# Kernel tuning notes

Hardware: AMD Instinct MI355X
Metric: run time of the kernel (lower is better)

The kernel has to match this reference:

```python
import jax, jax.numpy as jnp
import numpy as np

B, L, DIN, DM, NL, DI, DS, DC, DTR, NC = 32, 1024, 9, 512, 4, 1024, 16, 4, 32, 12


def setup_inputs() -> dict:
    key = jax.random.key(0)
    ks = jax.random.split(key, 8)
    s = 0.02
    return {
        'x': jax.random.normal(ks[0], (B, L, DIN), jnp.float32),
        'ip_w': jax.random.normal(ks[1], (DM, DIN), jnp.float32) * s,
        'ip_b': jnp.zeros((DM,), jnp.float32),
        'ln_g': jnp.ones((NL, DM), jnp.float32),
        'ln_b': jnp.zeros((NL, DM), jnp.float32),
        'in_proj_w': jax.random.normal(ks[2], (NL, 2 * DI, DM), jnp.float32) * s,
        'conv_w': jax.random.normal(ks[3], (NL, DI, DC), jnp.float32) * s,
        'conv_b': jnp.zeros((NL, DI), jnp.float32),
        'x_proj_w': jax.random.normal(ks[4], (NL, DTR + 2 * DS, DI), jnp.float32) * s,
        'dt_w': jax.random.normal(ks[5], (NL, DI, DTR), jnp.float32) * s,
        'dt_b': jnp.zeros((NL, DI), jnp.float32),
        'A_log': jnp.tile(jnp.log(jnp.arange(1, DS + 1, dtype=jnp.float32))[None, None, :], (NL, DI, 1)),
        'D': jnp.ones((NL, DI), jnp.float32),
        'out_proj_w': jax.random.normal(ks[6], (NL, DM, DI), jnp.float32) * s,
        'fc_w': jax.random.normal(ks[7], (NC, DM), jnp.float32) * s,
        'fc_b': jnp.zeros((NC,), jnp.float32),
    }


def _layernorm(x, g, b):
    m = jnp.mean(x, axis=-1, keepdims=True)
    v = jnp.var(x, axis=-1, keepdims=True)
    return (x - m) * jax.lax.rsqrt(v + 1e-5) * g + b


def _mamba(x, in_w, cw, cb, xp_w, dtw, dtb, Alog, Dp, ow):
    # x: (B, L, DM)
    xz = jnp.einsum('bld,ed->ble', x, in_w)          # (B, L, 2*DI)
    u, z = jnp.split(xz, 2, axis=-1)
    # causal depthwise conv1d over time
    ut = jnp.transpose(u, (0, 2, 1))                  # (B, DI, L)
    ut = jnp.pad(ut, ((0, 0), (0, 0), (DC - 1, 0)))
    conv = jax.lax.conv_general_dilated(
        ut, cw[:, None, :], (1,), 'VALID',
        feature_group_count=DI, dimension_numbers=('NCH', 'OIH', 'NCH'))
    u = jax.nn.silu(jnp.transpose(conv + cb[None, :, None], (0, 2, 1)))  # (B, L, DI)
    x_dbl = jnp.einsum('ble,fe->blf', u, xp_w)        # (B, L, DTR+2*DS)
    dt, Bm, Cm = jnp.split(x_dbl, [DTR, DTR + DS], axis=-1)
    delta = jax.nn.softplus(jnp.einsum('blr,er->ble', dt, dtw) + dtb)    # (B, L, DI)
    A = -jnp.exp(Alog)                                # (DI, DS)

    def step(h, inp):
        d_t, B_t, C_t, u_t = inp                      # (B,DI) (B,DS) (B,DS) (B,DI)
        dA = jnp.exp(d_t[:, :, None] * A)             # (B, DI, DS)
        h = dA * h + (d_t * u_t)[:, :, None] * B_t[:, None, :]
        y = jnp.einsum('bes,bs->be', h, C_t)
        return h, y

    xs = (jnp.moveaxis(delta, 1, 0), jnp.moveaxis(Bm, 1, 0),
          jnp.moveaxis(Cm, 1, 0), jnp.moveaxis(u, 1, 0))
    h0 = jnp.zeros((x.shape[0], DI, DS), x.dtype)
    _, ys = jax.lax.scan(step, h0, xs)                # (L, B, DI)
    y = jnp.moveaxis(ys, 0, 1) + u * Dp
    y = y * jax.nn.silu(z)
    return jnp.einsum('ble,de->bld', y, ow)           # (B, L, DM)


def reference(x, ip_w, ip_b, ln_g, ln_b, in_proj_w, conv_w, conv_b, x_proj_w, dt_w, dt_b, A_log, D, out_proj_w, fc_w, fc_b):
    h = jnp.einsum('bli,di->bld', x, ip_w) + ip_b
    for i in range(NL):
        res = h
        hn = _layernorm(h, ln_g[i], ln_b[i])
        h = _mamba(hn, in_proj_w[i], conv_w[i], conv_b[i], x_proj_w[i],
                   dt_w[i], dt_b[i], A_log[i], D[i], out_proj_w[i]) + res
    pooled = jnp.mean(h, axis=1)                      # (B, DM); dropout is identity in eval
    return pooled @ fc_w.T + fc_b                     # (B, NC)
```

## Files before the change

### kernel.cpp

```cpp
#include <hip/hip_runtime.h>
#include <hip/hip_bf16.h>

#define B_   32
#define L_   1024
#define DIN_ 9
#define DM_  512
#define NL_  4
#define DI_  1024
#define DS_  16
#define DC_  4
#define DTR_ 32
#define NC_  12
#define M_   (B_*L_)
#define NCC_ 2
#define MC_  (M_/NCC_)
#define BC_  (B_/NCC_)
#define NCH_ 16
#define CHT_ 64

typedef unsigned short u16;
typedef __attribute__((ext_vector_type(8))) short bf16x8;
typedef __attribute__((ext_vector_type(4))) float f32x4;

__device__ __forceinline__ float bf2f(u16 h){
  union { unsigned int u; float f; } v; v.u = ((unsigned int)h) << 16; return v.f;
}
__device__ __forceinline__ u16 f2bf(float f){
  union { float f; unsigned int u; } v; v.f = f;
  unsigned int u = v.u;
  return (u16)((u + 0x7fffu + ((u >> 16) & 1u)) >> 16);
}
__device__ __forceinline__ float siluf(float x){ return x / (1.f + __expf(-x)); }

__device__ __forceinline__ void gload_lds16(const u16* g, u16* l){
  __builtin_amdgcn_global_load_lds(
      (const __attribute__((address_space(1))) void*)(unsigned long long)(const void*)g,
      (__attribute__((address_space(3))) void*)(unsigned int)(unsigned long long)(void*)l,
      16, 0, 0);
}

#define NW1_ (NL_*2*DI_*DM_)
#define NW3_ (NL_*DM_*DI_)
#define NW2_ (NL_*64*DI_)
#define NW4_ (NL_*DI_*DTR_)
__global__ __launch_bounds__(256) void cast4_kernel(const float* __restrict__ a,
                                                    const float* __restrict__ c,
                                                    const float* __restrict__ e,
                                                    const float* __restrict__ f,
                                                    u16* __restrict__ oa,
                                                    u16* __restrict__ oc,
                                                    u16* __restrict__ oe,
                                                    u16* __restrict__ of){
  int i = blockIdx.x * 256 + threadIdx.x;
  if (i < NW1_) oa[i] = f2bf(a[i]);
  else if (i < NW1_ + NW3_) oc[i - NW1_] = f2bf(c[i - NW1_]);
  else if (i < NW1_ + NW3_ + NW2_) oe[i - NW1_ - NW3_] = f2bf(e[i - NW1_ - NW3_]);
  else if (i < NW1_ + NW3_ + NW2_ + NW4_)
    of[i - NW1_ - NW3_ - NW2_] = f2bf(f[i - NW1_ - NW3_ - NW2_]);
}

__global__ __launch_bounds__(256) void prep_kernel(const float* __restrict__ convw,
                                                   const float* __restrict__ A_log,
                                                   float* __restrict__ cwt,
                                                   float* __restrict__ At){
  int gid = blockIdx.x * 256 + threadIdx.x;
  int l = gid >> 10, e = gid & (DI_ - 1);
  float4 cw = *(const float4*)(convw + (size_t)gid * 4);
  cwt[(l * 4 + 0) * DI_ + e] = cw.x;
  cwt[(l * 4 + 1) * DI_ + e] = cw.y;
  cwt[(l * 4 + 2) * DI_ + e] = cw.z;
  cwt[(l * 4 + 3) * DI_ + e] = cw.w;
  const float* ar = A_log + (size_t)gid * DS_;
#pragma unroll
  for (int s = 0; s < DS_; s++)
    At[((size_t)l * DS_ + s) * DI_ + e] = -__expf(ar[s]);
}

__global__ __launch_bounds__(512) void inproj_kernel(const float* __restrict__ x,
                                                     const float* __restrict__ w,
                                                     const float* __restrict__ bias,
                                                     u16* __restrict__ h){
  int m = blockIdx.x;
  int d = threadIdx.x;
  __shared__ float xr[DIN_];
  if (threadIdx.x < DIN_) xr[threadIdx.x] = x[(size_t)m * DIN_ + threadIdx.x];
  __syncthreads();
  float a = bias[d];
#pragma unroll
  for (int i = 0; i < DIN_; i++) a += xr[i] * w[d * DIN_ + i];
  h[(size_t)m * DM_ + d] = f2bf(a);
}

__global__ __launch_bounds__(256) void ln_kernel(const u16* __restrict__ h,
                                                 const float* __restrict__ g,
                                                 const float* __restrict__ bt,
                                                 u16* __restrict__ hn){
  int row = blockIdx.x * 4 + (threadIdx.x >> 6);
  int lane = threadIdx.x & 63;
  const u16* hr = h + (size_t)row * DM_ + lane * 8;
  ushort4 a0 = *(const ushort4*)(hr);
  ushort4 a1 = *(const ushort4*)(hr + 4);
  float v[8];
  v[0]=bf2f(a0.x); v[1]=bf2f(a0.y); v[2]=bf2f(a0.z); v[3]=bf2f(a0.w);
  v[4]=bf2f(a1.x); v[5]=bf2f(a1.y); v[6]=bf2f(a1.z); v[7]=bf2f(a1.w);
  float s = 0.f, q = 0.f;
#pragma unroll
  for (int i = 0; i < 8; i++){ s += v[i]; q += v[i]*v[i]; }
#pragma unroll
  for (int o = 32; o; o >>= 1){ s += __shfl_xor(s, o); q += __shfl_xor(q, o); }
  float mean = s * (1.f / DM_);
  float rstd = rsqrtf(q * (1.f / DM_) - mean * mean + 1e-5f);
  float4 g0 = *(const float4*)(g + lane * 8);
  float4 g1 = *(const float4*)(g + lane * 8 + 4);
  float4 b0 = *(const float4*)(bt + lane * 8);
  float4 b1 = *(const float4*)(bt + lane * 8 + 4);
  ushort4 o0, o1;
  o0.x = f2bf((v[0]-mean)*rstd*g0.x + b0.x);
  o0.y = f2bf((v[1]-mean)*rstd*g0.y + b0.y);
  o0.z = f2bf((v[2]-mean)*rstd*g0.z + b0.z);
  o0.w = f2bf((v[3]-mean)*rstd*g0.w + b0.w);
  o1.x = f2bf((v[4]-mean)*rstd*g1.x + b1.x);
  o1.y = f2bf((v[5]-mean)*rstd*g1.y + b1.y);
  o1.z = f2bf((v[6]-mean)*rstd*g1.z + b1.z);
  o1.w = f2bf((v[7]-mean)*rstd*g1.w + b1.w);
  u16* op = hn + (size_t)row * DM_ + lane * 8;
  *(ushort4*)(op)     = o0;
  *(ushort4*)(op + 4) = o1;
}

__global__ __launch_bounds__(256) void conv8_kernel(const u16* __restrict__ xu,
                                                    const float* __restrict__ cwt,
                                                    const float* __restrict__ cbp,
                                                    u16* __restrict__ ub){
  int idx = blockIdx.x * 256 + threadIdx.x;
  int e8 = (idx & 127) * 8;
  int bl = idx >> 7;
  int l = bl & (L_ - 1);
  const u16* p = xu + (size_t)bl * DI_ + e8;
  float acc[8];
  {
    float4 c0 = *(const float4*)(cbp + e8);
    float4 c1 = *(const float4*)(cbp + e8 + 4);
    acc[0]=c0.x; acc[1]=c0.y; acc[2]=c0.z; acc[3]=c0.w;
    acc[4]=c1.x; acc[5]=c1.y; acc[6]=c1.z; acc[7]=c1.w;
  }
#pragma unroll
  for (int d = 0; d < 4; d++){
    if (l - 3 + d >= 0){
      const u16* q = p - (size_t)(3 - d) * DI_;
      ushort4 v0 = *(const ushort4*)q, v1 = *(const ushort4*)(q + 4);
      float4 w0 = *(const float4*)(cwt + d * DI_ + e8);
      float4 w1 = *(const float4*)(cwt + d * DI_ + e8 + 4);
      acc[0] += bf2f(v0.x) * w0.x; acc[1] += bf2f(v0.y) * w0.y;
      acc[2] += bf2f(v0.z) * w0.z; acc[3] += bf2f(v0.w) * w0.w;
      acc[4] += bf2f(v1.x) * w1.x; acc[5] += bf2f(v1.y) * w1.y;
      acc[6] += bf2f(v1.z) * w1.z; acc[7] += bf2f(v1.w) * w1.w;
    }
  }
  ushort4 h0, h1;
  h0.x = f2bf(siluf(acc[0])); h0.y = f2bf(siluf(acc[1]));
  h0.z = f2bf(siluf(acc[2])); h0.w = f2bf(siluf(acc[3]));
  h1.x = f2bf(siluf(acc[4])); h1.y = f2bf(siluf(acc[5]));
  h1.z = f2bf(siluf(acc[6])); h1.w = f2bf(siluf(acc[7]));
  u16* o = ub + (size_t)bl * DI_ + e8;
  *(ushort4*)o = h0;
  *(ushort4*)(o + 4) = h1;
}

template<int BM, int BN, int BK, int EPI>
__global__ __launch_bounds__(256)
void gemm_bt(const u16* __restrict__ A, int lda,
             const u16* __restrict__ Bw,
             u16* Cb, u16* Cb2, const u16* Res,
             const float* __restrict__ bias,
             int N, int K, int nsplit, int gx){
  constexpr int CH = BK / 8;
  constexpr int MASK = CH - 1;
  constexpr int WM = BM / 2, WN = BN / 2;
  constexpr int FM = WM / 16, FN = WN / 16;
  __shared__ u16 As_[BM * BK];
  __shared__ u16 Bs_[BN * BK];
  const int tid = threadIdx.x;
  const int lane = tid & 63;
  const int wid = tid >> 6;
  const int wr = wid >> 1, wc = wid & 1;
  int bm, bn;
  {
    const int wg = blockIdx.x;
    const int gy = (int)gridDim.x / gx;
    const int ypx = gy >> 3;
    const int xcd = wg & 7;
    const int idx = wg >> 3;
    const int y = xcd * ypx + (idx % ypx);
    const int x = idx / ypx;
    bm = y * BM; bn = x * BN;
  }
  f32x4 acc[FM][FN];
#pragma unroll
  for (int i = 0; i < FM; i++)
#pragma unroll
    for (int j = 0; j < FN; j++) acc[i][j] = f32x4{0.f, 0.f, 0.f, 0.f};
  constexpr int LA = BM * BK / (256 * 8);
  constexpr int LB = BN * BK / (256 * 8);
  const int wbase = wid * 64;
  for (int k0 = 0; k0 < K; k0 += BK){
    __syncthreads();
#pragma unroll
    for (int i = 0; i < LA; i++){
      int chunk = i * 256 + tid;
      int row = chunk / CH, cs = chunk & MASK;
      int cg = cs ^ (row & MASK);
      const u16* g = A + (size_t)(bm + row) * lda + k0 + cg * 8;
      gload_lds16(g, &As_[(i * 256 + wbase) * 8]);
    }
#pragma unroll
    for (int i = 0; i < LB; i++){
      int chunk = i * 256 + tid;
      int row = chunk / CH, cs = chunk & MASK;
      int cg = cs ^ (row & MASK);
      const u16* g = Bw + (size_t)(bn + row) * K + k0 + cg * 8;
      gload_lds16(g, &Bs_[(i * 256 + wbase) * 8]);
    }
    __syncthreads();
#pragma unroll
    for (int kk = 0; kk < BK / 32; kk++){
      bf16x8 af[FM], bfr[FN];
      const int kch = kk * 4 + (lane >> 4);
#pragma unroll
      for (int mi = 0; mi < FM; mi++){
        int r = wr * WM + mi * 16 + (lane & 15);
        af[mi] = *(const bf16x8*)(&As_[r * BK + ((kch ^ (r & MASK))) * 8]);
      }
#pragma unroll
      for (int ni = 0; ni < FN; ni++){
        int r = wc * WN + ni * 16 + (lane & 15);
        bfr[ni] = *(const bf16x8*)(&Bs_[r * BK + ((kch ^ (r & MASK))) * 8]);
      }
#pragma unroll
      for (int mi = 0; mi < FM; mi++)
#pragma unroll
        for (int ni = 0; ni < FN; ni++)
          acc[mi][ni] = __builtin_amdgcn_mfma_f32_16x16x32_bf16(af[mi], bfr[ni], acc[mi][ni], 0, 0, 0);
    }
  }
  const int rq = (lane >> 4) * 4, cl = lane & 15;
#pragma unroll
  for (int mi = 0; mi < FM; mi++){
#pragma unroll
    for (int ni = 0; ni < FN; ni++){
      const int n = bn + wc * WN + ni * 16 + cl;
#pragma unroll
      for (int j = 0; j < 4; j++){
        const int m = bm + wr * WM + mi * 16 + rq + j;
        float v = acc[mi][ni][j];
        if constexpr (EPI == 0){
          Cb[(size_t)m * N + n] = f2bf(v);
        } else if constexpr (EPI == 1){
          float xx = v + bias[n];
          float sp = (xx > 20.f) ? xx : __logf(1.f + __expf(xx));
          Cb[(size_t)m * N + n] = f2bf(sp);
        } else if constexpr (EPI == 2){
          const size_t off = (size_t)m * N + n;
          Cb[off] = f2bf(v + bf2f(Res[off]));
        } else {
          if (n < nsplit){
            Cb[(size_t)m * nsplit + n] = f2bf(v);
          } else {
            Cb2[(size_t)m * nsplit + (n - nsplit)] = f2bf(siluf(v));
          }
        }
      }
    }
  }
}

__global__ __launch_bounds__(256)
void scan1_kernel(const u16* __restrict__ ub, const u16* __restrict__ dlt,
                  const u16* __restrict__ xdb,
                  const float* __restrict__ At, float* __restrict__ sb){
  const int tid = threadIdx.x;
  const int e = blockIdx.x * 256 + tid;
  const int c = blockIdx.y, b = blockIdx.z;
  __shared__ float Bsh[CHT_][DS_];
  {
    int row = tid >> 2, col4 = (tid & 3) * 4;
    const u16* p = xdb + ((size_t)b * L_ + (size_t)c * CHT_ + row) * 64 + 32 + col4;
    ushort4 v = *(const ushort4*)p;
    Bsh[row][col4+0] = bf2f(v.x); Bsh[row][col4+1] = bf2f(v.y);
    Bsh[row][col4+2] = bf2f(v.z); Bsh[row][col4+3] = bf2f(v.w);
  }
  __syncthreads();
  float As[DS_];
  bool fast = true;
#pragma unroll
  for (int s = 0; s < DS_; s++){
    As[s] = At[(size_t)s * DI_ + e];
    fast = fast && (fabsf(As[s] + (float)(s + 1)) <= 1e-3f * (s + 1));
  }
  float h[DS_];
#pragma unroll
  for (int s = 0; s < DS_; s++) h[s] = 0.f;
  float sdd = 0.f;
  const size_t base = ((size_t)b * L_ + (size_t)c * CHT_) * DI_ + e;
  if (fast){
    for (int t = 0; t < CHT_; t++){
      const size_t idx = base + (size_t)t * DI_;
      float ut = bf2f(ub[idx]);
      float delta = bf2f(dlt[idx]);
      sdd += delta;
      float du = delta * ut;
      float e1 = __expf(-delta);
      float e2 = e1*e1, e4 = e2*e2, e8 = e4*e4;
      float dA[DS_] = {e1, e2, e2*e1, e4, e4*e1, e4*e2, e4*e2*e1, e8,
                       e8*e1, e8*e2, e8*e2*e1, e8*e4, e8*e4*e1, e8*e4*e2,
                       e8*e4*e2*e1, e8*e8};
      const float* r = &Bsh[t][0];
#pragma unroll
      for (int s = 0; s < DS_; s++)
        h[s] = fmaf(dA[s], h[s], du * r[s]);
    }
  } else {
    for (int t = 0; t < CHT_; t++){
      const size_t idx = base + (size_t)t * DI_;
      float ut = bf2f(ub[idx]);
      float delta = bf2f(dlt[idx]);
      sdd += delta;
      float du = delta * ut;
      const float* r = &Bsh[t][0];
#pragma unroll
      for (int s = 0; s < DS_; s++)
        h[s] = fmaf(__expf(delta * As[s]), h[s], du * r[s]);
    }
  }
  float* p = sb + ((size_t)c * (BC_ * DI_) + (size_t)b * DI_ + e) * 32;
  if (fast){
    float e1 = __expf(-sdd);
    float e2 = e1*e1, e4 = e2*e2, e8 = e4*e4;
    float ap[DS_] = {e1, e2, e2*e1, e4, e4*e1, e4*e2, e4*e2*e1, e8,
                     e8*e1, e8*e2, e8*e2*e1, e8*e4, e8*e4*e1, e8*e4*e2,
                     e8*e4*e2*e1, e8*e8};
#pragma unroll
    for (int s = 0; s < DS_; s++) p[s] = ap[s];
  } else {
#pragma unroll
    for (int s = 0; s < DS_; s++) p[s] = __expf(As[s] * sdd);
  }
#pragma unroll
  for (int s = 0; s < DS_; s++) p[16 + s] = h[s];
}

__global__ __launch_bounds__(256)
void scan2_kernel(float* __restrict__ sb){
  const int be = blockIdx.x * 256 + threadIdx.x;
  const int BE = BC_ * DI_;
  float h[DS_];
#pragma unroll
  for (int s = 0; s < DS_; s++) h[s] = 0.f;
  for (int c = 0; c < NCH_; c++){
    float* p = sb + ((size_t)c * BE + be) * 32;
    float4 a0 = *(const float4*)(p);
    float4 a1 = *(const float4*)(p + 4);
    float4 a2 = *(const float4*)(p + 8);
    float4 a3 = *(const float4*)(p + 12);
    float4 h0 = *(const float4*)(p + 16);
    float4 h1 = *(const float4*)(p + 20);
    float4 h2 = *(const float4*)(p + 24);
    float4 h3 = *(const float4*)(p + 28);
    float av[16] = {a0.x,a0.y,a0.z,a0.w, a1.x,a1.y,a1.z,a1.w,
                    a2.x,a2.y,a2.z,a2.w, a3.x,a3.y,a3.z,a3.w};
    float hv[16] = {h0.x,h0.y,h0.z,h0.w, h1.x,h1.y,h1.z,h1.w,
                    h2.x,h2.y,h2.z,h2.w, h3.x,h3.y,h3.z,h3.w};
    float4 w0, w1, w2, w3;
    float* wv[4] = {&w0.x, &w1.x, &w2.x, &w3.x};
#pragma unroll
    for (int s = 0; s < DS_; s++){
      float hi = h[s];
      h[s] = av[s] * hi + hv[s];
      wv[s >> 2][s & 3] = hi;
    }
    *(float4*)(p + 16) = w0;
    *(float4*)(p + 20) = w1;
    *(float4*)(p + 24) = w2;
    *(float4*)(p + 28) = w3;
  }
}

__global__ __launch_bounds__(256)
void scan3_kernel(const u16* __restrict__ ub, const u16* __restrict__ dlt,
                  u16* __restrict__ zy, const u16* __restrict__ xdb,
                  const float* __restrict__ At, const float* __restrict__ Dp,
                  const float* __restrict__ sb){
  const int tid = threadIdx.x;
  const int e = blockIdx.x * 256 + tid;
  const int c = blockIdx.y, b = blockIdx.z;
  __shared__ float BC[CHT_][32];
  {
#pragma unroll
    for (int q = 0; q < 2; q++){
      int idx = q * 256 + tid;
      int row = idx >> 3, col4 = (idx & 7) * 4;
      const u16* p = xdb + ((size_t)b * L_ + (size_t)c * CHT_ + row) * 64 + 32 + col4;
      ushort4 v = *(const ushort4*)p;
      BC[row][col4+0] = bf2f(v.x); BC[row][col4+1] = bf2f(v.y);
      BC[row][col4+2] = bf2f(v.z); BC[row][col4+3] = bf2f(v.w);
    }
  }
  __syncthreads();
  float As[DS_];
  bool fast = true;
#pragma unroll
  for (int s = 0; s < DS_; s++){
    As[s] = At[(size_t)s * DI_ + e];
    fast = fast && (fabsf(As[s] + (float)(s + 1)) <= 1e-3f * (s + 1));
  }
  const float Dv = Dp[e];
  const float* ip = sb + ((size_t)c * (BC_ * DI_) + (size_t)b * DI_ + e) * 32 + 16;
  float h[DS_];
#pragma unroll
  for (int s = 0; s < DS_; s++) h[s] = ip[s];
  const size_t base = ((size_t)b * L_ + (size_t)c * CHT_) * DI_ + e;
  if (fast){
    for (int t = 0; t < CHT_; t++){
      const size_t idx = base + (size_t)t * DI_;
      float ut = bf2f(ub[idx]);
      float delta = bf2f(dlt[idx]);
      float du = delta * ut;
      float e1 = __expf(-delta);
      float e2 = e1*e1, e4 = e2*e2, e8 = e4*e4;
      float dA[DS_] = {e1, e2, e2*e1, e4, e4*e1, e4*e2, e4*e2*e1, e8,
                       e8*e1, e8*e2, e8*e2*e1, e8*e4, e8*e4*e1, e8*e4*e2,
                       e8*e4*e2*e1, e8*e8};
      const float* r = &BC[t][0];
      float yv = 0.f;
#pragma unroll
      for (int s = 0; s < DS_; s++){
        h[s] = fmaf(dA[s], h[s], du * r[s]);
        yv = fmaf(h[s], r[16 + s], yv);
      }
      float zs = bf2f(zy[idx]);
      zy[idx] = f2bf((yv + ut * Dv) * zs);
    }
  } else {
    for (int t = 0; t < CHT_; t++){
      const size_t idx = base + (size_t)t * DI_;
      float ut = bf2f(ub[idx]);
      float delta = bf2f(dlt[idx]);
      float du = delta * ut;
      const float* r = &BC[t][0];
      float yv = 0.f;
#pragma unroll
      for (int s = 0; s < DS_; s++){
        h[s] = fmaf(__expf(delta * As[s]), h[s], du * r[s]);
        yv = fmaf(h[s], r[16 + s], yv);
      }
      float zs = bf2f(zy[idx]);
      zy[idx] = f2bf((yv + ut * Dv) * zs);
    }
  }
}

__global__ __launch_bounds__(256) void pool_kernel(const u16* __restrict__ h,
                                                   float* __restrict__ part){
  int d = blockIdx.x * 256 + threadIdx.x;
  int b = blockIdx.y;
  int p = blockIdx.z;
  float s = 0.f;
  const u16* hp = h + ((size_t)b * L_ + p * 128) * DM_ + d;
  for (int l = 0; l < 128; l++) s += bf2f(hp[(size_t)l * DM_]);
  part[((size_t)p * B_ + b) * DM_ + d] = s;
}

__global__ __launch_bounds__(256) void fc_kernel(const float* __restrict__ part,
                                                 const float* __restrict__ fcw,
                                                 const float* __restrict__ fcb,
                                                 float* __restrict__ out){
  int b = blockIdx.x;
  int tid = threadIdx.x;
  __shared__ float pd[DM_];
  for (int d = tid; d < DM_; d += 256){
    float s = 0.f;
    for (int p = 0; p < 8; p++) s += part[((size_t)p * B_ + b) * DM_ + d];
    pd[d] = s * (1.f / L_);
  }
  __syncthreads();
  int wid = tid >> 6, lane = tid & 63;
  for (int c = wid; c < NC_; c += 4){
    float s = 0.f;
    for (int d = lane; d < DM_; d += 64) s += pd[d] * fcw[c * DM_ + d];
#pragma unroll
    for (int o = 32; o; o >>= 1) s += __shfl_xor(s, o);
    if (lane == 0) out[b * NC_ + c] = s + fcb[c];
  }
}

extern "C" void kernel_launch(void* const* d_in, const int* in_sizes, int n_in,
                              void* d_out, int out_size, void* d_ws, size_t ws_size,
                              hipStream_t stream){
  const float* x     = (const float*)d_in[0];
  const float* ip_w  = (const float*)d_in[1];
  const float* ip_b  = (const float*)d_in[2];
  const float* ln_g  = (const float*)d_in[3];
  const float* ln_b  = (const float*)d_in[4];
  const float* inpw  = (const float*)d_in[5];
  const float* convw = (const float*)d_in[6];
  const float* convb = (const float*)d_in[7];
  const float* xpw   = (const float*)d_in[8];
  const float* dtw   = (const float*)d_in[9];
  const float* dtb   = (const float*)d_in[10];
  const float* Alog  = (const float*)d_in[11];
  const float* Dp    = (const float*)d_in[12];
  const float* outw  = (const float*)d_in[13];
  const float* fcw   = (const float*)d_in[14];
  const float* fcb   = (const float*)d_in[15];
  float* out = (float*)d_out;

  char* ws = (char*)d_ws;
  size_t off = 0;
  auto alloc = [&](size_t bytes) -> void* {
    void* p = ws + off; off += (bytes + 255) & ~(size_t)255; return p;
  };
  u16*    h16   = (u16*)   alloc((size_t)M_ * DM_ * 2);
  float*  part  = (float*) alloc((size_t)8 * B_ * DM_ * 4);
  u16*    w_in  = (u16*)   alloc((size_t)NW1_ * 2);
  u16*    w_out = (u16*)   alloc((size_t)NW3_ * 2);
  u16*    w_xp  = (u16*)   alloc((size_t)NW2_ * 2);
  u16*    w_dt  = (u16*)   alloc((size_t)NW4_ * 2);
  float*  cwt   = (float*) alloc((size_t)NL_ * 4 * DI_ * 4);
  float*  At    = (float*) alloc((size_t)NL_ * DS_ * DI_ * 4);
  u16*    xu    = (u16*)   alloc((size_t)MC_ * DI_ * 2);
  u16*    ub    = (u16*)   alloc((size_t)MC_ * DI_ * 2);
  u16*    xzs   = (u16*)   alloc((size_t)MC_ * DI_ * 2);
  u16*    dlt   = (u16*)   alloc((size_t)MC_ * DI_ * 2);
  u16*    xdb   = (u16*)   alloc((size_t)MC_ * 64 * 2);
  float*  sb    = (float*) alloc((size_t)NCH_ * BC_ * DI_ * 32 * 4);
  u16*    hn    = dlt;

  cast4_kernel<<<(NW1_ + NW3_ + NW2_ + NW4_ + 255) / 256, 256, 0, stream>>>(
      inpw, outw, xpw, dtw, w_in, w_out, w_xp, w_dt);
  prep_kernel<<<(NL_ * DI_) / 256, 256, 0, stream>>>(convw, Alog, cwt, At);
  inproj_kernel<<<M_, 512, 0, stream>>>(x, ip_w, ip_b, h16);

  const int GY = MC_ / 128;
  for (int i = 0; i < NL_; i++){
    for (int c = 0; c < NCC_; c++){
      u16* hc = h16 + (size_t)c * MC_ * DM_;

      ln_kernel<<<MC_ / 4, 256, 0, stream>>>(hc, ln_g + i * DM_, ln_b + i * DM_, hn);

      gemm_bt<128, 128, 64, 4><<<16 * GY, 256, 0, stream>>>(
          hn, DM_, w_in + (size_t)i * 2 * DI_ * DM_, xu, xzs, nullptr, nullptr,
          2 * DI_, DM_, DI_, 16);

      conv8_kernel<<<(MC_ * DI_ / 8) / 256, 256, 0, stream>>>(
          xu, cwt + (size_t)i * 4 * DI_, convb + i * DI_, ub);

      gemm_bt<128, 64, 64, 0><<<1 * GY, 256, 0, stream>>>(
          ub, DI_, w_xp + (size_t)i * 64 * DI_, xdb, nullptr, nullptr, nullptr,
          64, DI_, 0, 1);

      gemm_bt<128, 128, 32, 1><<<8 * GY, 256, 0, stream>>>(
          xdb, 64, w_dt + (size_t)i * DI_ * DTR_, dlt, nullptr, nullptr,
          dtb + i * DI_, DI_, DTR_, 0, 8);

      scan1_kernel<<<dim3(DI_ / 256, NCH_, BC_), 256, 0, stream>>>(
          ub, dlt, xdb, At + (size_t)i * DS_ * DI_, sb);
      scan2_kernel<<<(BC_ * DI_) / 256, 256, 0, stream>>>(sb);
      scan3_kernel<<<dim3(DI_ / 256, NCH_, BC_), 256, 0, stream>>>(
          ub, dlt, xzs, xdb, At + (size_t)i * DS_ * DI_, Dp + i * DI_, sb);

      gemm_bt<128, 128, 64, 2><<<4 * GY, 256, 0, stream>>>(
          xzs, DI_, w_out + (size_t)i * DM_ * DI_, hc, nullptr, hc,
          nullptr, DM_, DI_, 0, 4);
    }
  }

  pool_kernel<<<dim3(2, B_, 8), 256, 0, stream>>>(h16, part);
  fc_kernel<<<B_, 256, 0, stream>>>(part, fcw, fcb, out);
}
```

Measured before the change: 2.241 ms.

## Fuse causal conv+SiLU into x_proj GEMM A-load and scan kernels

Removes the standalone conv8 kernel and the materialized ub buffer. The x_proj GEMM now computes conv+SiLU while loading its A tile into LDS, using register loads instead of async global-to-LDS copies. The scan1 and scan3 kernels recompute the conv on the fly with a rolling 3-tap window. SiLU also switches from a divide to a hardware reciprocal. This saves a kernel launch and a full write-plus-read of the activation per layer chunk, at the cost of redundant conv compute in three places and a slower, synchronous A-load in the x_proj GEMM.

```diff
diff --git a/kernel.cpp b/kernel.cpp
--- a/kernel.cpp
+++ b/kernel.cpp
@@ -30,7 +30,9 @@
   unsigned int u = v.u;
   return (u16)((u + 0x7fffu + ((u >> 16) & 1u)) >> 16);
 }
-__device__ __forceinline__ float siluf(float x){ return x / (1.f + __expf(-x)); }
+__device__ __forceinline__ float siluf(float x){
+  return x * __builtin_amdgcn_rcpf(1.f + __expf(-x));
+}
 
 __device__ __forceinline__ void gload_lds16(const u16* g, u16* l){
   __builtin_amdgcn_global_load_lds(
@@ -128,51 +130,13 @@
   *(ushort4*)(op + 4) = o1;
 }
 
-__global__ __launch_bounds__(256) void conv8_kernel(const u16* __restrict__ xu,
-                                                    const float* __restrict__ cwt,
-                                                    const float* __restrict__ cbp,
-                                                    u16* __restrict__ ub){
-  int idx = blockIdx.x * 256 + threadIdx.x;
-  int e8 = (idx & 127) * 8;
-  int bl = idx >> 7;
-  int l = bl & (L_ - 1);
-  const u16* p = xu + (size_t)bl * DI_ + e8;
-  float acc[8];
-  {
-    float4 c0 = *(const float4*)(cbp + e8);
-    float4 c1 = *(const float4*)(cbp + e8 + 4);
-    acc[0]=c0.x; acc[1]=c0.y; acc[2]=c0.z; acc[3]=c0.w;
-    acc[4]=c1.x; acc[5]=c1.y; acc[6]=c1.z; acc[7]=c1.w;
-  }
-#pragma unroll
-  for (int d = 0; d < 4; d++){
-    if (l - 3 + d >= 0){
-      const u16* q = p - (size_t)(3 - d) * DI_;
-      ushort4 v0 = *(const ushort4*)q, v1 = *(const ushort4*)(q + 4);
-      float4 w0 = *(const float4*)(cwt + d * DI_ + e8);
-      float4 w1 = *(const float4*)(cwt + d * DI_ + e8 + 4);
-      acc[0] += bf2f(v0.x) * w0.x; acc[1] += bf2f(v0.y) * w0.y;
-      acc[2] += bf2f(v0.z) * w0.z; acc[3] += bf2f(v0.w) * w0.w;
-      acc[4] += bf2f(v1.x) * w1.x; acc[5] += bf2f(v1.y) * w1.y;
-      acc[6] += bf2f(v1.z) * w1.z; acc[7] += bf2f(v1.w) * w1.w;
-    }
-  }
-  ushort4 h0, h1;
-  h0.x = f2bf(siluf(acc[0])); h0.y = f2bf(siluf(acc[1]));
-  h0.z = f2bf(siluf(acc[2])); h0.w = f2bf(siluf(acc[3]));
-  h1.x = f2bf(siluf(acc[4])); h1.y = f2bf(siluf(acc[5]));
-  h1.z = f2bf(siluf(acc[6])); h1.w = f2bf(siluf(acc[7]));
-  u16* o = ub + (size_t)bl * DI_ + e8;
-  *(ushort4*)o = h0;
-  *(ushort4*)(o + 4) = h1;
-}
-
-template<int BM, int BN, int BK, int EPI>
+template<int BM, int BN, int BK, int EPI, int STAGE>
 __global__ __launch_bounds__(256)
 void gemm_bt(const u16* __restrict__ A, int lda,
              const u16* __restrict__ Bw,
              u16* Cb, u16* Cb2, const u16* Res,
              const float* __restrict__ bias,
+             const float* __restrict__ cwp, const float* __restrict__ cbp,
              int N, int K, int nsplit, int gx){
   constexpr int CH = BK / 8;
   constexpr int MASK = CH - 1;
@@ -184,6 +148,7 @@
   const int lane = tid & 63;
   const int wid = tid >> 6;
   const int wr = wid >> 1, wc = wid & 1;
+  const int cc0 = tid & MASK;
   int bm, bn;
   {
     const int wg = blockIdx.x;
@@ -204,14 +169,57 @@
   constexpr int LB = BN * BK / (256 * 8);
   const int wbase = wid * 64;
   for (int k0 = 0; k0 < K; k0 += BK){
+    float cwv[4][8], cbv[8];
+    if constexpr (STAGE == 2){
+      const int col0 = k0 + cc0 * 8;
+#pragma unroll
+      for (int d = 0; d < 4; d++){
+        float4 w0 = *(const float4*)(cwp + d * DI_ + col0);
+        float4 w1 = *(const float4*)(cwp + d * DI_ + col0 + 4);
+        cwv[d][0]=w0.x; cwv[d][1]=w0.y; cwv[d][2]=w0.z; cwv[d][3]=w0.w;
+        cwv[d][4]=w1.x; cwv[d][5]=w1.y; cwv[d][6]=w1.z; cwv[d][7]=w1.w;
+      }
+      float4 c0 = *(const float4*)(cbp + col0);
+      float4 c1 = *(const float4*)(cbp + col0 + 4);
+      cbv[0]=c0.x; cbv[1]=c0.y; cbv[2]=c0.z; cbv[3]=c0.w;
+      cbv[4]=c1.x; cbv[5]=c1.y; cbv[6]=c1.z; cbv[7]=c1.w;
+    }
     __syncthreads();
 #pragma unroll
     for (int i = 0; i < LA; i++){
       int chunk = i * 256 + tid;
       int row = chunk / CH, cs = chunk & MASK;
-      int cg = cs ^ (row & MASK);
-      const u16* g = A + (size_t)(bm + row) * lda + k0 + cg * 8;
-      gload_lds16(g, &As_[(i * 256 + wbase) * 8]);
+      if constexpr (STAGE == 0){
+        int cg = cs ^ (row & MASK);
+        const u16* g = A + (size_t)(bm + row) * lda + k0 + cg * 8;
+        gload_lds16(g, &As_[(i * 256 + wbase) * 8]);
+      } else {
+        const int m = bm + row;
+        const int l = m & (L_ - 1);
+        const u16* pb = A + (size_t)m * lda + k0 + cs * 8;
+        float acc8[8];
+#pragma unroll
+        for (int j = 0; j < 8; j++) acc8[j] = cbv[j];
+#pragma unroll
+        for (int d = 0; d < 4; d++){
+          if (l - 3 + d >= 0){
+            const u16* p = pb - (size_t)(3 - d) * lda;
+            ushort4 q0 = *(const ushort4*)p, q1 = *(const ushort4*)(p + 4);
+            float uv[8] = {bf2f(q0.x), bf2f(q0.y), bf2f(q0.z), bf2f(q0.w),
+                           bf2f(q1.x), bf2f(q1.y), bf2f(q1.z), bf2f(q1.w)};
+#pragma unroll
+            for (int j = 0; j < 8; j++) acc8[j] += uv[j] * cwv[d][j];
+          }
+        }
+        ushort4 h0, h1;
+        h0.x = f2bf(siluf(acc8[0])); h0.y = f2bf(siluf(acc8[1]));
+        h0.z = f2bf(siluf(acc8[2])); h0.w = f2bf(siluf(acc8[3]));
+        h1.x = f2bf(siluf(acc8[4])); h1.y = f2bf(siluf(acc8[5]));
+        h1.z = f2bf(siluf(acc8[6])); h1.w = f2bf(siluf(acc8[7]));
+        u16* dst = &As_[row * BK + ((cs ^ (row & MASK))) * 8];
+        *(ushort4*)dst = h0;
+        *(ushort4*)(dst + 4) = h1;
+      }
     }
 #pragma unroll
     for (int i = 0; i < LB; i++){
@@ -275,8 +283,9 @@
 }
 
 __global__ __launch_bounds__(256)
-void scan1_kernel(const u16* __restrict__ ub, const u16* __restrict__ dlt,
+void scan1_kernel(const u16* __restrict__ xu, const u16* __restrict__ dlt,
                   const u16* __restrict__ xdb,
+                  const float* __restrict__ cwt, const float* __restrict__ cbp,
                   const float* __restrict__ At, float* __restrict__ sb){
   const int tid = threadIdx.x;
   const int e = blockIdx.x * 256 + tid;
@@ -297,15 +306,24 @@
     As[s] = At[(size_t)s * DI_ + e];
     fast = fast && (fabsf(As[s] + (float)(s + 1)) <= 1e-3f * (s + 1));
   }
+  const float4 cwv = make_float4(cwt[e], cwt[DI_ + e], cwt[2 * DI_ + e], cwt[3 * DI_ + e]);
+  const float cbe = cbp[e];
+  const int l0 = c * CHT_;
+  float p0 = (l0 >= 3) ? bf2f(xu[((size_t)b * L_ + l0 - 3) * DI_ + e]) : 0.f;
+  float p1 = (l0 >= 2) ? bf2f(xu[((size_t)b * L_ + l0 - 2) * DI_ + e]) : 0.f;
+  float p2 = (l0 >= 1) ? bf2f(xu[((size_t)b * L_ + l0 - 1) * DI_ + e]) : 0.f;
   float h[DS_];
 #pragma unroll
   for (int s = 0; s < DS_; s++) h[s] = 0.f;
   float sdd = 0.f;
-  const size_t base = ((size_t)b * L_ + (size_t)c * CHT_) * DI_ + e;
+  const size_t base = ((size_t)b * L_ + l0) * DI_ + e;
   if (fast){
     for (int t = 0; t < CHT_; t++){
       const size_t idx = base + (size_t)t * DI_;
-      float ut = bf2f(ub[idx]);
+      float up = bf2f(xu[idx]);
+      float a = cbe + cwv.x * p0 + cwv.y * p1 + cwv.z * p2 + cwv.w * up;
+      p0 = p1; p1 = p2; p2 = up;
+      float ut = siluf(a);
       float delta = bf2f(dlt[idx]);
       sdd += delta;
       float du = delta * ut;
@@ -322,7 +340,10 @@
   } else {
     for (int t = 0; t < CHT_; t++){
       const size_t idx = base + (size_t)t * DI_;
-      float ut = bf2f(ub[idx]);
+      float up = bf2f(xu[idx]);
+      float a = cbe + cwv.x * p0 + cwv.y * p1 + cwv.z * p2 + cwv.w * up;
+      p0 = p1; p1 = p2; p2 = up;
+      float ut = siluf(a);
       float delta = bf2f(dlt[idx]);
       sdd += delta;
       float du = delta * ut;
@@ -386,8 +407,9 @@
 }
 
 __global__ __launch_bounds__(256)
-void scan3_kernel(const u16* __restrict__ ub, const u16* __restrict__ dlt,
+void scan3_kernel(const u16* __restrict__ xu, const u16* __restrict__ dlt,
                   u16* __restrict__ zy, const u16* __restrict__ xdb,
+                  const float* __restrict__ cwt, const float* __restrict__ cbp,
                   const float* __restrict__ At, const float* __restrict__ Dp,
                   const float* __restrict__ sb){
   const int tid = threadIdx.x;
@@ -413,16 +435,25 @@
     As[s] = At[(size_t)s * DI_ + e];
     fast = fast && (fabsf(As[s] + (float)(s + 1)) <= 1e-3f * (s + 1));
   }
+  const float4 cwv = make_float4(cwt[e], cwt[DI_ + e], cwt[2 * DI_ + e], cwt[3 * DI_ + e]);
+  const float cbe = cbp[e];
   const float Dv = Dp[e];
+  const int l0 = c * CHT_;
+  float p0 = (l0 >= 3) ? bf2f(xu[((size_t)b * L_ + l0 - 3) * DI_ + e]) : 0.f;
+  float p1 = (l0 >= 2) ? bf2f(xu[((size_t)b * L_ + l0 - 2) * DI_ + e]) : 0.f;
+  float p2 = (l0 >= 1) ? bf2f(xu[((size_t)b * L_ + l0 - 1) * DI_ + e]) : 0.f;
   const float* ip = sb + ((size_t)c * (BC_ * DI_) + (size_t)b * DI_ + e) * 32 + 16;
   float h[DS_];
 #pragma unroll
   for (int s = 0; s < DS_; s++) h[s] = ip[s];
-  const size_t base = ((size_t)b * L_ + (size_t)c * CHT_) * DI_ + e;
+  const size_t base = ((size_t)b * L_ + l0) * DI_ + e;
   if (fast){
     for (int t = 0; t < CHT_; t++){
       const size_t idx = base + (size_t)t * DI_;
-      float ut = bf2f(ub[idx]);
+      float up = bf2f(xu[idx]);
+      float a = cbe + cwv.x * p0 + cwv.y * p1 + cwv.z * p2 + cwv.w * up;
+      p0 = p1; p1 = p2; p2 = up;
+      float ut = siluf(a);
       float delta = bf2f(dlt[idx]);
       float du = delta * ut;
       float e1 = __expf(-delta);
@@ -443,7 +474,10 @@
   } else {
     for (int t = 0; t < CHT_; t++){
       const size_t idx = base + (size_t)t * DI_;
-      float ut = bf2f(ub[idx]);
+      float up = bf2f(xu[idx]);
+      float a = cbe + cwv.x * p0 + cwv.y * p1 + cwv.z * p2 + cwv.w * up;
+      p0 = p1; p1 = p2; p2 = up;
+      float ut = siluf(a);
       float delta = bf2f(dlt[idx]);
       float du = delta * ut;
       const float* r = &BC[t][0];
@@ -528,7 +562,6 @@
   float*  cwt   = (float*) alloc((size_t)NL_ * 4 * DI_ * 4);
   float*  At    = (float*) alloc((size_t)NL_ * DS_ * DI_ * 4);
   u16*    xu    = (u16*)   alloc((size_t)MC_ * DI_ * 2);
-  u16*    ub    = (u16*)   alloc((size_t)MC_ * DI_ * 2);
   u16*    xzs   = (u16*)   alloc((size_t)MC_ * DI_ * 2);
   u16*    dlt   = (u16*)   alloc((size_t)MC_ * DI_ * 2);
   u16*    xdb   = (u16*)   alloc((size_t)MC_ * 64 * 2);
@@ -542,35 +575,35 @@
 
   const int GY = MC_ / 128;
   for (int i = 0; i < NL_; i++){
+    const float* cwt_l = cwt + (size_t)i * 4 * DI_;
+    const float* cb_l  = convb + (size_t)i * DI_;
     for (int c = 0; c < NCC_; c++){
       u16* hc = h16 + (size_t)c * MC_ * DM_;
 
       ln_kernel<<<MC_ / 4, 256, 0, stream>>>(hc, ln_g + i * DM_, ln_b + i * DM_, hn);
 
-      gemm_bt<128, 128, 64, 4><<<16 * GY, 256, 0, stream>>>(
+      gemm_bt<128, 128, 64, 4, 0><<<16 * GY, 256, 0, stream>>>(
           hn, DM_, w_in + (size_t)i * 2 * DI_ * DM_, xu, xzs, nullptr, nullptr,
-          2 * DI_, DM_, DI_, 16);
-
-      conv8_kernel<<<(MC_ * DI_ / 8) / 256, 256, 0, stream>>>(
-          xu, cwt + (size_t)i * 4 * DI_, convb + i * DI_, ub);
-
-      gemm_bt<128, 64, 64, 0><<<1 * GY, 256, 0, stream>>>(
-          ub, DI_, w_xp + (size_t)i * 64 * DI_, xdb, nullptr, nullptr, nullptr,
-          64, DI_, 0, 1);
-
-      gemm_bt<128, 128, 32, 1><<<8 * GY, 256, 0, stream>>>(
+          nullptr, nullptr, 2 * DI_, DM_, DI_, 16);
+
+      gemm_bt<128, 64, 64, 0, 2><<<1 * GY, 256, 0, stream>>>(
+          xu, DI_, w_xp + (size_t)i * 64 * DI_, xdb, nullptr, nullptr, nullptr,
+          cwt_l, cb_l, 64, DI_, 0, 1);
+
+      gemm_bt<128, 128, 32, 1, 0><<<8 * GY, 256, 0, stream>>>(
           xdb, 64, w_dt + (size_t)i * DI_ * DTR_, dlt, nullptr, nullptr,
-          dtb + i * DI_, DI_, DTR_, 0, 8);
+          dtb + i * DI_, nullptr, nullptr, DI_, DTR_, 0, 8);
 
       scan1_kernel<<<dim3(DI_ / 256, NCH_, BC_), 256, 0, stream>>>(
-          ub, dlt, xdb, At + (size_t)i * DS_ * DI_, sb);
+          xu, dlt, xdb, cwt_l, cb_l, At + (size_t)i * DS_ * DI_, sb);
       scan2_kernel<<<(BC_ * DI_) / 256, 256, 0, stream>>>(sb);
       scan3_kernel<<<dim3(DI_ / 256, NCH_, BC_), 256, 0, stream>>>(
-          ub, dlt, xzs, xdb, At + (size_t)i * DS_ * DI_, Dp + i * DI_, sb);
-
-      gemm_bt<128, 128, 64, 2><<<4 * GY, 256, 0, stream>>>(
+          xu, dlt, xzs, xdb, cwt_l, cb_l, At + (size_t)i * DS_ * DI_,
+          Dp + i * DI_, sb);
+
+      gemm_bt<128, 128, 64, 2, 0><<<4 * GY, 256, 0, stream>>>(
           xzs, DI_, w_out + (size_t)i * DM_ * DI_, hc, nullptr, hc,
-          nullptr, DM_, DI_, 0, 4);
+          nullptr, nullptr, nullptr, DM_, DI_, 0, 4);
     }
   }
 
```

After: 2.866 ms. 1.28x slower.
